# Performance work log

Measured on AMD Instinct MI355X. Metric: run time of the kernel, lower is better.

The kernel has to match this reference:

```python
import jax, jax.numpy as jnp
import numpy as np

EPS = 1e-5
B, N, K = 2, 20000, 17      # batch, num points, k+1 neighbors
CIN = 128                   # bn_size * growth_rate
G = 128                     # growth_rate


def index_points(pts, idx):
    # pts: [B, C, N], idx: [B, S, K] -> [B, C, S, K]
    return jnp.take_along_axis(pts[:, :, :, None], idx[:, None, :, :], axis=2)


def conv_bn_relu(x, W, b, gamma, beta, mean, var):
    # 1x1 Conv2d + BatchNorm2d (inference, running stats) + ReLU
    # x: [B, Cin, N, K], W: [Cout, Cin]
    y = jnp.einsum('oc,bcnk->bonk', W, x) + b[None, :, None, None]
    inv = gamma / jnp.sqrt(var + EPS)
    y = y * inv[None, :, None, None] + (beta - mean * inv)[None, :, None, None]
    return jax.nn.relu(y)


def setup_inputs() -> dict:
    key = jax.random.key(0)
    ks = jax.random.split(key, 16)
    feats = jax.random.normal(ks[0], (B, CIN, N), dtype=jnp.float32)
    pts = jax.random.normal(ks[1], (B, 3, N), dtype=jnp.float32)
    knn_idx = jax.random.randint(ks[2], (B, N, K), 0, N, dtype=jnp.int32)
    s = 0.05
    d = {
        'feats': feats, 'pts': pts, 'knn_idx': knn_idx,
        'Wd': jax.random.normal(ks[3], (G, 3), dtype=jnp.float32) * s,
        'bd': jnp.zeros((G,), jnp.float32),
        'gd': jnp.ones((G,), jnp.float32),
        'betad': jnp.zeros((G,), jnp.float32),
        'md': jax.random.normal(ks[4], (G,), dtype=jnp.float32) * 0.01,
        'vd': jax.random.uniform(ks[5], (G,), jnp.float32, 0.5, 1.5),
        'Wf': jax.random.normal(ks[6], (G, CIN), dtype=jnp.float32) * s,
        'bf': jnp.zeros((G,), jnp.float32),
        'gf': jnp.ones((G,), jnp.float32),
        'betaf': jnp.zeros((G,), jnp.float32),
        'mf': jax.random.normal(ks[7], (G,), dtype=jnp.float32) * 0.01,
        'vf': jax.random.uniform(ks[8], (G,), jnp.float32, 0.5, 1.5),
        'Wp': jax.random.normal(ks[9], (G, G), dtype=jnp.float32) * s,
        'bp': jnp.zeros((G,), jnp.float32),
        'gp': jnp.ones((G,), jnp.float32),
        'betap': jnp.zeros((G,), jnp.float32),
        'mp': jax.random.normal(ks[10], (G,), dtype=jnp.float32) * 0.01,
        'vp': jax.random.uniform(ks[11], (G,), jnp.float32, 0.5, 1.5),
    }
    return d


def reference(feats, pts, knn_idx,
              Wd, bd, gd, betad, md, vd,
              Wf, bf, gf, betaf, mf, vf,
              Wp, bp, gp, betap, mp, vp):
    # Point3DConv.forward with precomputed knn_idx
    knn_pts = index_points(pts, knn_idx)                 # [B,3,N,K]
    knn_delta = knn_pts - pts[:, :, :, None]             # [B,3,N,K]
    knn_delta = conv_bn_relu(knn_delta, Wd, bd, gd, betad, md, vd)   # [B,G,N,K]
    knn_feats = index_points(feats, knn_idx)              # [B,CIN,N,K]
    knn_feats = conv_bn_relu(knn_feats, Wf, bf, gf, betaf, mf, vf)   # [B,G,N,K]
    new_feats = knn_delta * knn_feats                     # [B,G,N,K]
    new_feats = conv_bn_relu(new_feats, Wp, bp, gp, betap, mp, vp)   # [B,G,N,K]
    return new_feats.sum(axis=-1)                         # [B,G,N]
```

## Files before the change

### kernel.cpp

```cpp
#include <hip/hip_runtime.h>
#include <hip/hip_bf16.h>
#include <cstdint>
#include <cstddef>

#define NB 2
#define NPT 20000
#define KNN 17
#define CH 128
#define NT16 (NPT/16)
#define NT32 (NPT/32)
#define EPSV 1e-5f

typedef short short8 __attribute__((ext_vector_type(8)));
typedef float f32x4 __attribute__((ext_vector_type(4)));

__device__ __forceinline__ unsigned short f2bf(float x) {
    union { float f; unsigned int u; } v; v.f = x;
    unsigned int r = v.u + 0x7FFFu + ((v.u >> 16) & 1u);
    return (unsigned short)(r >> 16);
}
__device__ __forceinline__ float bf_lo(unsigned w) {
    union { unsigned u; float f; } v; v.u = w << 16; return v.f;
}
__device__ __forceinline__ float bf_hi(unsigned w) {
    union { unsigned u; float f; } v; v.u = w & 0xffff0000u; return v.f;
}
__device__ __forceinline__ unsigned pack_bf2(float a, float b) {
    __hip_bfloat162 h2 = __float22bfloat162_rn(make_float2(a, b));
    union { __hip_bfloat162 h; unsigned u; } cv; cv.h = h2; return cv.u;
}

__global__ __launch_bounds__(256) void k_feats(
    const float* __restrict__ feats, const float* __restrict__ Wf,
    const float* __restrict__ bfv, const float* __restrict__ gf,
    const float* __restrict__ betaf, const float* __restrict__ mf,
    const float* __restrict__ vf, unsigned short* __restrict__ Fout)
{
    __shared__ unsigned short A_lds[32][136];
    __shared__ unsigned short O_lds[32][136];
    const int t  = threadIdx.x;
    const int b  = blockIdx.x / NT32;
    const int n0 = (blockIdx.x % NT32) * 32;

    {
        const int chunk = t & 7;
        const int cbase = t >> 3;
        const float* base = feats + (size_t)b*CH*NPT + n0 + chunk*4;
        #pragma unroll
        for (int it = 0; it < 4; ++it) {
            int c = it*32 + cbase;
            float4 v = *(const float4*)(base + (size_t)c*NPT);
            A_lds[chunk*4+0][c] = f2bf(v.x);
            A_lds[chunk*4+1][c] = f2bf(v.y);
            A_lds[chunk*4+2][c] = f2bf(v.z);
            A_lds[chunk*4+3][c] = f2bf(v.w);
        }
    }

    const int lane = t & 63, wid = t >> 6;
    const int h = lane >> 4, r16 = lane & 15;
    const int gb = wid * 32;

    short8 bfrag[2][4];
    float sf[2], tf[2];
    #pragma unroll
    for (int T = 0; T < 2; ++T) {
        int g = gb + T*16 + r16;
        #pragma unroll
        for (int s = 0; s < 4; ++s) {
            const float* wrow = Wf + g*CH + s*32 + h*8;
            float4 w0 = *(const float4*)(wrow);
            float4 w1 = *(const float4*)(wrow + 4);
            short8 f;
            f[0]=(short)f2bf(w0.x); f[1]=(short)f2bf(w0.y);
            f[2]=(short)f2bf(w0.z); f[3]=(short)f2bf(w0.w);
            f[4]=(short)f2bf(w1.x); f[5]=(short)f2bf(w1.y);
            f[6]=(short)f2bf(w1.z); f[7]=(short)f2bf(w1.w);
            bfrag[T][s] = f;
        }
        float inv = gf[g] * rsqrtf(vf[g] + EPSV);
        sf[T] = inv;
        tf[T] = bfv[g]*inv + betaf[g] - mf[g]*inv;
    }
    __syncthreads();

    #pragma unroll
    for (int sub = 0; sub < 2; ++sub) {
        #pragma unroll
        for (int T = 0; T < 2; ++T) {
            f32x4 acc = {0.f, 0.f, 0.f, 0.f};
            #pragma unroll
            for (int s = 0; s < 4; ++s) {
                short8 a = *(const short8*)&A_lds[sub*16 + r16][s*32 + h*8];
                acc = __builtin_amdgcn_mfma_f32_16x16x32_bf16(a, bfrag[T][s], acc, 0, 0, 0);
            }
            #pragma unroll
            for (int r = 0; r < 4; ++r) {
                float y = fmaxf(fmaf(sf[T], acc[r], tf[T]), 0.f);
                O_lds[sub*16 + 4*h + r][gb + T*16 + r16] = f2bf(y);
            }
        }
    }
    __syncthreads();

    {
        const int pp = t >> 3, cc = (t & 7) * 16;
        uint4 v0 = *(const uint4*)&O_lds[pp][cc];
        uint4 v1 = *(const uint4*)&O_lds[pp][cc + 8];
        unsigned short* dst = Fout + ((size_t)b*NPT + n0 + pp)*CH + cc;
        *(uint4*)dst = v0;
        *(uint4*)(dst + 8) = v1;
    }
}

struct Pref { float dx, dy, dz; uint4 fr; };

__device__ __forceinline__ Pref issueK(const int* __restrict__ idx_lds, int p_t, int k,
    const float* __restrict__ px, const float* __restrict__ py,
    const float* __restrict__ pz, const unsigned short* __restrict__ Fb, int c0)
{
    Pref P;
    int nb = idx_lds[p_t*KNN + k];
    P.dx = px[nb]; P.dy = py[nb]; P.dz = pz[nb];
    P.fr = *(const uint4*)(Fb + (size_t)nb*CH + c0);
    return P;
}

__device__ __forceinline__ void stageRow(unsigned short (*A)[136], int p_t, int c0,
    const float4* dcf, const float* tq, const Pref& P)
{
    unsigned fw0 = P.fr.x, fw1 = P.fr.y, fw2 = P.fr.z, fw3 = P.fr.w;
    float pr[8];
    const unsigned fws[4] = {fw0, fw1, fw2, fw3};
    #pragma unroll
    for (int q = 0; q < 8; ++q) {
        float d = fmaf(dcf[q].x, P.dx, fmaf(dcf[q].y, P.dy, fmaf(dcf[q].z, P.dz, tq[q])));
        d = fmaxf(d, 0.f);
        float f = (q & 1) ? bf_hi(fws[q >> 1]) : bf_lo(fws[q >> 1]);
        pr[q] = d * f;
    }
    uint4 pack;
    pack.x = pack_bf2(pr[0], pr[1]);
    pack.y = pack_bf2(pr[2], pr[3]);
    pack.z = pack_bf2(pr[4], pr[5]);
    pack.w = pack_bf2(pr[6], pr[7]);
    *(uint4*)&A[p_t][c0] = pack;
}

__device__ __forceinline__ void mfmaPlane(const unsigned short (*A)[136], int r16, int h,
    const short8 bfrag[2][4], const float* sp, const float* tp, f32x4* facc)
{
    #pragma unroll
    for (int T = 0; T < 2; ++T) {
        f32x4 acc = {0.f, 0.f, 0.f, 0.f};
        #pragma unroll
        for (int s = 0; s < 4; ++s) {
            short8 a = *(const short8*)&A[r16][s*32 + h*8];
            acc = __builtin_amdgcn_mfma_f32_16x16x32_bf16(a, bfrag[T][s], acc, 0, 0, 0);
        }
        #pragma unroll
        for (int r = 0; r < 4; ++r)
            facc[T][r] += fmaxf(fmaf(sp[T], acc[r], tp[T]), 0.f);
    }
}

__global__ __launch_bounds__(256) void k_main(
    const float* __restrict__ pts, const int* __restrict__ knn,
    const unsigned short* __restrict__ F,
    const float* __restrict__ Wd, const float* __restrict__ bd,
    const float* __restrict__ gd, const float* __restrict__ betad,
    const float* __restrict__ md, const float* __restrict__ vd,
    const float* __restrict__ Wp, const float* __restrict__ bp,
    const float* __restrict__ gp, const float* __restrict__ betap,
    const float* __restrict__ mp, const float* __restrict__ vp,
    float* __restrict__ out)
{
    __shared__ unsigned short A2[2][16][136];
    __shared__ int   idx_lds[16*KNN];
    __shared__ float4 dcoef[CH];

    const int t  = threadIdx.x;
    const int b  = blockIdx.x / NT16;
    const int n0 = (blockIdx.x % NT16) * 16;

    for (int e = t; e < 16*KNN; e += 256)
        idx_lds[e] = knn[((size_t)b*NPT + n0)*KNN + e];
    if (t < CH) {
        float inv = gd[t] * rsqrtf(vd[t] + EPSV);
        float td  = bd[t]*inv + betad[t] - md[t]*inv;
        dcoef[t]  = make_float4(Wd[t*3]*inv, Wd[t*3+1]*inv, Wd[t*3+2]*inv, td);
    }
    __syncthreads();

    const int p_t = t >> 4, c0 = (t & 15) * 8;
    const int lane = t & 63, wid = t >> 6;
    const int h = lane >> 4, r16 = lane & 15;
    const int gb = wid * 32;

    const float* px = pts + (size_t)b*3*NPT;
    const float* py = px + NPT;
    const float* pz = py + NPT;
    const unsigned short* Fb = F + (size_t)b*NPT*CH;

    Pref PA = issueK(idx_lds, p_t, 0, px, py, pz, Fb, c0);
    Pref PB = issueK(idx_lds, p_t, 1, px, py, pz, Fb, c0);

    short8 bfrag[2][4];
    float sp[2], tp[2];
    #pragma unroll
    for (int T = 0; T < 2; ++T) {
        int g = gb + T*16 + r16;
        #pragma unroll
        for (int s = 0; s < 4; ++s) {
            const float* wrow = Wp + g*CH + s*32 + h*8;
            float4 w0 = *(const float4*)(wrow);
            float4 w1 = *(const float4*)(wrow + 4);
            short8 f;
            f[0]=(short)f2bf(w0.x); f[1]=(short)f2bf(w0.y);
            f[2]=(short)f2bf(w0.z); f[3]=(short)f2bf(w0.w);
            f[4]=(short)f2bf(w1.x); f[5]=(short)f2bf(w1.y);
            f[6]=(short)f2bf(w1.z); f[7]=(short)f2bf(w1.w);
            bfrag[T][s] = f;
        }
        float inv = gp[g] * rsqrtf(vp[g] + EPSV);
        sp[T] = inv;
        tp[T] = bp[g]*inv + betap[g] - mp[g]*inv;
    }

    float4 dcf[8];
    float  tq[8];
    {
        float cx = px[n0 + p_t], cy = py[n0 + p_t], cz = pz[n0 + p_t];
        #pragma unroll
        for (int q = 0; q < 8; ++q) {
            dcf[q] = dcoef[c0 + q];
            tq[q]  = dcf[q].w - (dcf[q].x*cx + dcf[q].y*cy + dcf[q].z*cz);
        }
    }

    f32x4 facc[2] = {{0.f,0.f,0.f,0.f},{0.f,0.f,0.f,0.f}};

    stageRow(A2[0], p_t, c0, dcf, tq, PA);
    PA = issueK(idx_lds, p_t, 2, px, py, pz, Fb, c0);
    __syncthreads();

    #pragma unroll 1
    for (int k = 0; k < 16; k += 2) {
        mfmaPlane(A2[0], r16, h, bfrag, sp, tp, facc);
        stageRow(A2[1], p_t, c0, dcf, tq, PB);
        if (k + 3 < KNN) PB = issueK(idx_lds, p_t, k+3, px, py, pz, Fb, c0);
        __syncthreads();
        mfmaPlane(A2[1], r16, h, bfrag, sp, tp, facc);
        stageRow(A2[0], p_t, c0, dcf, tq, PA);
        if (k + 4 < KNN) PA = issueK(idx_lds, p_t, k+4, px, py, pz, Fb, c0);
        __syncthreads();
    }
    mfmaPlane(A2[0], r16, h, bfrag, sp, tp, facc);

    #pragma unroll
    for (int T = 0; T < 2; ++T) {
        int g = gb + T*16 + r16;
        *(f32x4*)(out + ((size_t)b*CH + g)*NPT + n0 + 4*h) = facc[T];
    }
}

extern "C" void kernel_launch(void* const* d_in, const int* in_sizes, int n_in,
                              void* d_out, int out_size, void* d_ws, size_t ws_size,
                              hipStream_t stream)
{
    const float* feats = (const float*)d_in[0];
    const float* pts   = (const float*)d_in[1];
    const int*   knn   = (const int*)d_in[2];
    const float* Wd    = (const float*)d_in[3];
    const float* bd    = (const float*)d_in[4];
    const float* gd    = (const float*)d_in[5];
    const float* betad = (const float*)d_in[6];
    const float* md    = (const float*)d_in[7];
    const float* vd    = (const float*)d_in[8];
    const float* Wf    = (const float*)d_in[9];
    const float* bfv   = (const float*)d_in[10];
    const float* gf    = (const float*)d_in[11];
    const float* betaf = (const float*)d_in[12];
    const float* mf    = (const float*)d_in[13];
    const float* vf    = (const float*)d_in[14];
    const float* Wp    = (const float*)d_in[15];
    const float* bp    = (const float*)d_in[16];
    const float* gp    = (const float*)d_in[17];
    const float* betap = (const float*)d_in[18];
    const float* mp    = (const float*)d_in[19];
    const float* vp    = (const float*)d_in[20];
    float* out = (float*)d_out;
    unsigned short* Fws = (unsigned short*)d_ws;

    k_feats<<<dim3(NB * NT32), 256, 0, stream>>>(feats, Wf, bfv, gf, betaf, mf, vf, Fws);
    k_main <<<dim3(NB * NT16), 256, 0, stream>>>(pts, knn, Fws, Wd, bd, gd, betad, md, vd,
                                                 Wp, bp, gp, betap, mp, vp, out);
}
```

Measured before the change: 78.37 us.

## Process two neighbor planes per barrier and vectorize elementwise math as float2

```diff
diff --git a/kernel.cpp b/kernel.cpp
--- a/kernel.cpp
+++ b/kernel.cpp
@@ -13,21 +13,29 @@
 
 typedef short short8 __attribute__((ext_vector_type(8)));
 typedef float f32x4 __attribute__((ext_vector_type(4)));
+typedef float f32x2 __attribute__((ext_vector_type(2)));
 
 __device__ __forceinline__ unsigned short f2bf(float x) {
     union { float f; unsigned int u; } v; v.f = x;
     unsigned int r = v.u + 0x7FFFu + ((v.u >> 16) & 1u);
     return (unsigned short)(r >> 16);
 }
-__device__ __forceinline__ float bf_lo(unsigned w) {
-    union { unsigned u; float f; } v; v.u = w << 16; return v.f;
-}
-__device__ __forceinline__ float bf_hi(unsigned w) {
-    union { unsigned u; float f; } v; v.u = w & 0xffff0000u; return v.f;
-}
 __device__ __forceinline__ unsigned pack_bf2(float a, float b) {
     __hip_bfloat162 h2 = __float22bfloat162_rn(make_float2(a, b));
     union { __hip_bfloat162 h; unsigned u; } cv; cv.h = h2; return cv.u;
+}
+__device__ __forceinline__ f32x2 bfpair(unsigned w) {
+    union { unsigned u; float f; } lo, hi;
+    lo.u = w << 16; hi.u = w & 0xffff0000u;
+    f32x2 r; r[0] = lo.f; r[1] = hi.f; return r;
+}
+__device__ __forceinline__ short8 packrow(const float* wrow) {
+    float4 w0 = *(const float4*)(wrow);
+    float4 w1 = *(const float4*)(wrow + 4);
+    uint4 uu;
+    uu.x = pack_bf2(w0.x, w0.y); uu.y = pack_bf2(w0.z, w0.w);
+    uu.z = pack_bf2(w1.x, w1.y); uu.w = pack_bf2(w1.z, w1.w);
+    union { uint4 u; short8 s; } cv; cv.u = uu; return cv.s;
 }
 
 __global__ __launch_bounds__(256) void k_feats(
@@ -67,17 +75,8 @@
     for (int T = 0; T < 2; ++T) {
         int g = gb + T*16 + r16;
         #pragma unroll
-        for (int s = 0; s < 4; ++s) {
-            const float* wrow = Wf + g*CH + s*32 + h*8;
-            float4 w0 = *(const float4*)(wrow);
-            float4 w1 = *(const float4*)(wrow + 4);
-            short8 f;
-            f[0]=(short)f2bf(w0.x); f[1]=(short)f2bf(w0.y);
-            f[2]=(short)f2bf(w0.z); f[3]=(short)f2bf(w0.w);
-            f[4]=(short)f2bf(w1.x); f[5]=(short)f2bf(w1.y);
-            f[6]=(short)f2bf(w1.z); f[7]=(short)f2bf(w1.w);
-            bfrag[T][s] = f;
-        }
+        for (int s = 0; s < 4; ++s)
+            bfrag[T][s] = packrow(Wf + g*CH + s*32 + h*8);
         float inv = gf[g] * rsqrtf(vf[g] + EPSV);
         sf[T] = inv;
         tf[T] = bfv[g]*inv + betaf[g] - mf[g]*inv;
@@ -86,14 +85,16 @@
 
     #pragma unroll
     for (int sub = 0; sub < 2; ++sub) {
+        short8 a[4];
+        #pragma unroll
+        for (int s = 0; s < 4; ++s)
+            a[s] = *(const short8*)&A_lds[sub*16 + r16][s*32 + h*8];
         #pragma unroll
         for (int T = 0; T < 2; ++T) {
             f32x4 acc = {0.f, 0.f, 0.f, 0.f};
             #pragma unroll
-            for (int s = 0; s < 4; ++s) {
-                short8 a = *(const short8*)&A_lds[sub*16 + r16][s*32 + h*8];
-                acc = __builtin_amdgcn_mfma_f32_16x16x32_bf16(a, bfrag[T][s], acc, 0, 0, 0);
-            }
+            for (int s = 0; s < 4; ++s)
+                acc = __builtin_amdgcn_mfma_f32_16x16x32_bf16(a[s], bfrag[T][s], acc, 0, 0, 0);
             #pragma unroll
             for (int r = 0; r < 4; ++r) {
                 float y = fmaxf(fmaf(sf[T], acc[r], tf[T]), 0.f);
@@ -115,52 +116,56 @@
 
 struct Pref { float dx, dy, dz; uint4 fr; };
 
-__device__ __forceinline__ Pref issueK(const int* __restrict__ idx_lds, int p_t, int k,
+__device__ __forceinline__ Pref issueK(const int* __restrict__ idx_row, int k,
     const float* __restrict__ px, const float* __restrict__ py,
     const float* __restrict__ pz, const unsigned short* __restrict__ Fb, int c0)
 {
     Pref P;
-    int nb = idx_lds[p_t*KNN + k];
+    int nb = idx_row[k];
     P.dx = px[nb]; P.dy = py[nb]; P.dz = pz[nb];
     P.fr = *(const uint4*)(Fb + (size_t)nb*CH + c0);
     return P;
 }
 
 __device__ __forceinline__ void stageRow(unsigned short (*A)[136], int p_t, int c0,
-    const float4* dcf, const float* tq, const Pref& P)
-{
-    unsigned fw0 = P.fr.x, fw1 = P.fr.y, fw2 = P.fr.z, fw3 = P.fr.w;
-    float pr[8];
-    const unsigned fws[4] = {fw0, fw1, fw2, fw3};
-    #pragma unroll
-    for (int q = 0; q < 8; ++q) {
-        float d = fmaf(dcf[q].x, P.dx, fmaf(dcf[q].y, P.dy, fmaf(dcf[q].z, P.dz, tq[q])));
-        d = fmaxf(d, 0.f);
-        float f = (q & 1) ? bf_hi(fws[q >> 1]) : bf_lo(fws[q >> 1]);
-        pr[q] = d * f;
-    }
-    uint4 pack;
-    pack.x = pack_bf2(pr[0], pr[1]);
-    pack.y = pack_bf2(pr[2], pr[3]);
-    pack.z = pack_bf2(pr[4], pr[5]);
-    pack.w = pack_bf2(pr[6], pr[7]);
+    const f32x2* wx2, const f32x2* wy2, const f32x2* wz2, const f32x2* tq2,
+    const Pref& P)
+{
+    const unsigned fw[4] = {P.fr.x, P.fr.y, P.fr.z, P.fr.w};
+    const f32x2 zero2 = {0.f, 0.f};
+    unsigned pk[4];
+    #pragma unroll
+    for (int q = 0; q < 4; ++q) {
+        f32x2 d = wx2[q]*P.dx + wy2[q]*P.dy + wz2[q]*P.dz + tq2[q];
+        d = __builtin_elementwise_max(d, zero2);
+        f32x2 pr = d * bfpair(fw[q]);
+        pk[q] = pack_bf2(pr[0], pr[1]);
+    }
+    uint4 pack; pack.x = pk[0]; pack.y = pk[1]; pack.z = pk[2]; pack.w = pk[3];
     *(uint4*)&A[p_t][c0] = pack;
 }
 
 __device__ __forceinline__ void mfmaPlane(const unsigned short (*A)[136], int r16, int h,
-    const short8 bfrag[2][4], const float* sp, const float* tp, f32x4* facc)
-{
+    const short8 bfrag[2][4], const float* spv, const float* tpv, f32x2 facc2[2][2])
+{
+    short8 a[4];
+    #pragma unroll
+    for (int s = 0; s < 4; ++s)
+        a[s] = *(const short8*)&A[r16][s*32 + h*8];
+    const f32x2 zero2 = {0.f, 0.f};
     #pragma unroll
     for (int T = 0; T < 2; ++T) {
         f32x4 acc = {0.f, 0.f, 0.f, 0.f};
         #pragma unroll
-        for (int s = 0; s < 4; ++s) {
-            short8 a = *(const short8*)&A[r16][s*32 + h*8];
-            acc = __builtin_amdgcn_mfma_f32_16x16x32_bf16(a, bfrag[T][s], acc, 0, 0, 0);
+        for (int s = 0; s < 4; ++s)
+            acc = __builtin_amdgcn_mfma_f32_16x16x32_bf16(a[s], bfrag[T][s], acc, 0, 0, 0);
+        #pragma unroll
+        for (int half = 0; half < 2; ++half) {
+            f32x2 a2; a2[0] = acc[2*half]; a2[1] = acc[2*half+1];
+            f32x2 y = a2 * spv[T] + tpv[T];
+            y = __builtin_elementwise_max(y, zero2);
+            facc2[T][half] += y;
         }
-        #pragma unroll
-        for (int r = 0; r < 4; ++r)
-            facc[T][r] += fmaxf(fmaf(sp[T], acc[r], tp[T]), 0.f);
     }
 }
 
@@ -175,7 +180,7 @@
     const float* __restrict__ mp, const float* __restrict__ vp,
     float* __restrict__ out)
 {
-    __shared__ unsigned short A2[2][16][136];
+    __shared__ unsigned short A3[2][2][16][136];
     __shared__ int   idx_lds[16*KNN];
     __shared__ float4 dcoef[CH];
 
@@ -201,66 +206,73 @@
     const float* py = px + NPT;
     const float* pz = py + NPT;
     const unsigned short* Fb = F + (size_t)b*NPT*CH;
-
-    Pref PA = issueK(idx_lds, p_t, 0, px, py, pz, Fb, c0);
-    Pref PB = issueK(idx_lds, p_t, 1, px, py, pz, Fb, c0);
+    const int* idx_row = idx_lds + p_t*KNN;
+
+    Pref PA = issueK(idx_row, 0, px, py, pz, Fb, c0);
+    Pref PB = issueK(idx_row, 1, px, py, pz, Fb, c0);
 
     short8 bfrag[2][4];
-    float sp[2], tp[2];
+    float spv[2], tpv[2];
     #pragma unroll
     for (int T = 0; T < 2; ++T) {
         int g = gb + T*16 + r16;
         #pragma unroll
-        for (int s = 0; s < 4; ++s) {
-            const float* wrow = Wp + g*CH + s*32 + h*8;
-            float4 w0 = *(const float4*)(wrow);
-            float4 w1 = *(const float4*)(wrow + 4);
-            short8 f;
-            f[0]=(short)f2bf(w0.x); f[1]=(short)f2bf(w0.y);
-            f[2]=(short)f2bf(w0.z); f[3]=(short)f2bf(w0.w);
-            f[4]=(short)f2bf(w1.x); f[5]=(short)f2bf(w1.y);
-            f[6]=(short)f2bf(w1.z); f[7]=(short)f2bf(w1.w);
-            bfrag[T][s] = f;
-        }
+        for (int s = 0; s < 4; ++s)
+            bfrag[T][s] = packrow(Wp + g*CH + s*32 + h*8);
         float inv = gp[g] * rsqrtf(vp[g] + EPSV);
-        sp[T] = inv;
-        tp[T] = bp[g]*inv + betap[g] - mp[g]*inv;
-    }
-
-    float4 dcf[8];
-    float  tq[8];
+        spv[T] = inv;
+        tpv[T] = bp[g]*inv + betap[g] - mp[g]*inv;
+    }
+
+    f32x2 wx2[4], wy2[4], wz2[4], tq2[4];
     {
         float cx = px[n0 + p_t], cy = py[n0 + p_t], cz = pz[n0 + p_t];
         #pragma unroll
-        for (int q = 0; q < 8; ++q) {
-            dcf[q] = dcoef[c0 + q];
-            tq[q]  = dcf[q].w - (dcf[q].x*cx + dcf[q].y*cy + dcf[q].z*cz);
+        for (int q = 0; q < 4; ++q) {
+            float4 a = dcoef[c0 + 2*q];
+            float4 c = dcoef[c0 + 2*q + 1];
+            wx2[q][0] = a.x; wx2[q][1] = c.x;
+            wy2[q][0] = a.y; wy2[q][1] = c.y;
+            wz2[q][0] = a.z; wz2[q][1] = c.z;
+            tq2[q][0] = a.w - (a.x*cx + a.y*cy + a.z*cz);
+            tq2[q][1] = c.w - (c.x*cx + c.y*cy + c.z*cz);
         }
     }
 
-    f32x4 facc[2] = {{0.f,0.f,0.f,0.f},{0.f,0.f,0.f,0.f}};
-
-    stageRow(A2[0], p_t, c0, dcf, tq, PA);
-    PA = issueK(idx_lds, p_t, 2, px, py, pz, Fb, c0);
-    __syncthreads();
-
+    f32x2 facc2[2][2] = {{{0.f,0.f},{0.f,0.f}},{{0.f,0.f},{0.f,0.f}}};
+
+    stageRow(A3[0][0], p_t, c0, wx2, wy2, wz2, tq2, PA);
+    PA = issueK(idx_row, 2, px, py, pz, Fb, c0);
+    stageRow(A3[0][1], p_t, c0, wx2, wy2, wz2, tq2, PB);
+    PB = issueK(idx_row, 3, px, py, pz, Fb, c0);
+    __syncthreads();
+
+    int cur = 0;
     #pragma unroll 1
-    for (int k = 0; k < 16; k += 2) {
-        mfmaPlane(A2[0], r16, h, bfrag, sp, tp, facc);
-        stageRow(A2[1], p_t, c0, dcf, tq, PB);
-        if (k + 3 < KNN) PB = issueK(idx_lds, p_t, k+3, px, py, pz, Fb, c0);
+    for (int i = 0; i < 7; ++i) {
+        const int k = 2*i;
+        mfmaPlane(A3[cur][0], r16, h, bfrag, spv, tpv, facc2);
+        mfmaPlane(A3[cur][1], r16, h, bfrag, spv, tpv, facc2);
+        stageRow(A3[cur^1][0], p_t, c0, wx2, wy2, wz2, tq2, PA);
+        PA = issueK(idx_row, k+4, px, py, pz, Fb, c0);
+        stageRow(A3[cur^1][1], p_t, c0, wx2, wy2, wz2, tq2, PB);
+        if (k + 5 < KNN) PB = issueK(idx_row, k+5, px, py, pz, Fb, c0);
         __syncthreads();
-        mfmaPlane(A2[1], r16, h, bfrag, sp, tp, facc);
-        stageRow(A2[0], p_t, c0, dcf, tq, PA);
-        if (k + 4 < KNN) PA = issueK(idx_lds, p_t, k+4, px, py, pz, Fb, c0);
-        __syncthreads();
-    }
-    mfmaPlane(A2[0], r16, h, bfrag, sp, tp, facc);
+        cur ^= 1;
+    }
+    mfmaPlane(A3[cur][0], r16, h, bfrag, spv, tpv, facc2);
+    mfmaPlane(A3[cur][1], r16, h, bfrag, spv, tpv, facc2);
+    stageRow(A3[cur^1][0], p_t, c0, wx2, wy2, wz2, tq2, PA);
+    __syncthreads();
+    mfmaPlane(A3[cur^1][0], r16, h, bfrag, spv, tpv, facc2);
 
     #pragma unroll
     for (int T = 0; T < 2; ++T) {
         int g = gb + T*16 + r16;
-        *(f32x4*)(out + ((size_t)b*CH + g)*NPT + n0 + 4*h) = facc[T];
+        f32x4 o;
+        o[0] = facc2[T][0][0]; o[1] = facc2[T][0][1];
+        o[2] = facc2[T][1][0]; o[3] = facc2[T][1][1];
+        *(f32x4*)(out + ((size_t)b*CH + g)*NPT + n0 + 4*h) = o;
     }
 }
 
```

Measured after the change: 74.63 us. 1.05x faster.
